# Optimization experiments

Hardware: AMD Instinct MI355X
Metric: run time of the kernel (lower is better)

The kernel has to match this reference:

```python
import jax, jax.numpy as jnp
import numpy as np
import math

FEATURES = 1024; HEADS = 8; STATES = 64; DCONV = 4; EXPAND = 2; NGROUPS = 1; CHUNK = 256
INNER = EXPAND * FEATURES           # 2048
HALF = INNER // 2                   # 1024
HEADDIM = HALF // HEADS             # 128
CONVDIM = HALF + 2 * NGROUPS * STATES  # 1152
B = 2; L = 4096
EPS = 1e-5


def setup_inputs() -> dict:
    key = jax.random.key(0)
    ks = jax.random.split(key, 8)
    u = jax.random.normal(ks[0], (B, L, FEATURES), jnp.float32)
    W_in = jax.random.normal(ks[1], (FEATURES, INNER + 2 * NGROUPS * STATES + HEADS), jnp.float32) * (FEATURES ** -0.5)
    xconv_w = jax.random.normal(ks[2], (CONVDIM, DCONV), jnp.float32) * (DCONV ** -0.5)
    xconv_b = jnp.zeros((CONVDIM,), jnp.float32)
    zconv_w = jax.random.normal(ks[3], (HALF, DCONV), jnp.float32) * (DCONV ** -0.5)
    zconv_b = jnp.zeros((HALF,), jnp.float32)
    dt0 = jnp.exp(jax.random.uniform(ks[4], (HEADS,)) * (math.log(0.1) - math.log(0.001)) + math.log(0.001))
    dt0 = jnp.clip(dt0, 1e-4, None)
    dt_bias = dt0 + jnp.log(-jnp.expm1(-dt0))  # inverse-softplus init
    Alog = jnp.log(jax.random.uniform(ks[5], (HEADS,), minval=1.0, maxval=16.0))
    D = jnp.ones((HEADS,), jnp.float32)
    norm_w = jnp.ones((INNER,), jnp.float32)
    W_out = jax.random.normal(ks[6], (INNER, FEATURES), jnp.float32) * (INNER ** -0.5)
    return dict(u=u, W_in=W_in, xconv_w=xconv_w, xconv_b=xconv_b, zconv_w=zconv_w,
                zconv_b=zconv_b, dt_bias=dt_bias, Alog=Alog, D=D, norm_w=norm_w, W_out=W_out)


def _causal_dwconv_silu(x, w, b):
    # x: (B, L, C), w: (C, K) depthwise, b: (C,) -> causal conv + SiLU, (B, L, C)
    xt = jnp.transpose(x, (0, 2, 1))  # B C L
    kern = w[:, None, :]              # (C, 1, K) -> OIH with groups=C
    y = jax.lax.conv_general_dilated(xt, kern, window_strides=(1,),
                                     padding=[(w.shape[1] - 1, 0)],
                                     dimension_numbers=('NCH', 'OIH', 'NCH'),
                                     feature_group_count=w.shape[0])
    y = jax.nn.silu(y + b[None, :, None])
    return jnp.transpose(y, (0, 2, 1))


def _ssd(x, dt, A, Bm, Cm, Dp, chunk):
    # x:(b,l,h,p) dt:(b,l,h) A:(h,) Bm,Cm:(b,l,g,n) Dp:(h,)
    b, Ltot, H, P = x.shape
    G, N = Bm.shape[2], Bm.shape[3]
    nc = Ltot // chunk
    X = (x * dt[..., None]).reshape(b, nc, chunk, H, P)          # dt-scaled input
    Adt = jnp.transpose((dt * A[None, None, :]).reshape(b, nc, chunk, H), (0, 3, 1, 2))  # b h c k
    Bh = jnp.repeat(Bm, H // G, axis=2).reshape(b, nc, chunk, H, N)
    Ch = jnp.repeat(Cm, H // G, axis=2).reshape(b, nc, chunk, H, N)
    cs = jnp.cumsum(Adt, axis=-1)                                # b h c k
    seg = cs[..., :, None] - cs[..., None, :]                    # b h c l s
    mask = jnp.tril(jnp.ones((chunk, chunk), bool))
    Lmat = jnp.exp(jnp.where(mask, seg, -jnp.inf))               # causal decay matrix
    # intra-chunk (diagonal block) output
    Y_diag = jnp.einsum('bclhn,bcshn,bhcls,bcshp->bclhp', Ch, Bh, Lmat, X)
    # per-chunk final states
    decay_states = jnp.exp(cs[..., -1:] - cs)                    # b h c k
    states = jnp.einsum('bcshn,bhcs,bcshp->bchpn', Bh, decay_states, X)
    chunk_decay = jnp.exp(cs[..., -1])                           # b h c
    def step(carry, inp):
        s, d = inp
        return s + d[..., None, None] * carry, carry             # emit incoming state
    _, prev = jax.lax.scan(step, jnp.zeros((b, H, P, N), x.dtype),
                           (jnp.transpose(states, (1, 0, 2, 3, 4)),
                            jnp.transpose(chunk_decay, (2, 0, 1))))  # prev: (c,b,h,p,n)
    Y_off = jnp.einsum('bclhn,bhcl,cbhpn->bclhp', Ch, jnp.exp(cs), prev)
    Y = (Y_diag + Y_off).reshape(b, Ltot, H, P)
    return Y + Dp[None, None, :, None] * x                       # D skip uses raw x


def _forward(u, W_in, xconv_w, xconv_b, zconv_w, zconv_b, dt_bias, Alog, D, norm_w, W_out):
    zxbcdt = u @ W_in
    z = zxbcdt[..., :HALF]
    xBC = zxbcdt[..., HALF:HALF + CONVDIM]
    dt = jax.nn.softplus(zxbcdt[..., HALF + CONVDIM:] + dt_bias)  # (B,L,H)
    A = -jnp.exp(Alog)
    xBC = _causal_dwconv_silu(xBC, xconv_w, xconv_b)
    z = _causal_dwconv_silu(z, zconv_w, zconv_b)
    x = xBC[..., :HALF].reshape(B, L, HEADS, HEADDIM)
    Bm = xBC[..., HALF:HALF + NGROUPS * STATES].reshape(B, L, NGROUPS, STATES)
    Cm = xBC[..., HALF + NGROUPS * STATES:].reshape(B, L, NGROUPS, STATES)
    y = _ssd(x, dt, A, Bm, Cm, D, CHUNK).reshape(B, L, HALF)
    y = jnp.concatenate([y, z], axis=-1)                          # (B,L,INNER)
    y = y * jax.lax.rsqrt(jnp.mean(y * y, axis=-1, keepdims=True) + EPS) * norm_w
    return y @ W_out


def reference(u, W_in, xconv_w, xconv_b, zconv_w, zconv_b, dt_bias, Alog, D, norm_w, W_out):
    return _forward(u, W_in, xconv_w, xconv_b, zconv_w, zconv_b, dt_bias, Alog, D, norm_w, W_out)
```

## Files before the change

### kernel.cpp

```cpp
#include <hip/hip_runtime.h>
#include <stdint.h>

#define DEV __device__ __forceinline__

typedef __attribute__((ext_vector_type(8))) short bf16x8_t;
typedef __attribute__((ext_vector_type(4))) float f32x4_t;

DEV unsigned short f2bf(float f) {
  union { float f; uint32_t u; } x; x.f = f;
  uint32_t r = x.u + 0x7fffu + ((x.u >> 16) & 1u);
  return (unsigned short)(r >> 16);
}
DEV float bf2f(unsigned short u) {
  union { uint32_t u; float f; } x; x.u = ((uint32_t)u) << 16;
  return x.f;
}

#define GLOAD_LDS16(g, l)                                                              \
  __builtin_amdgcn_global_load_lds((const __attribute__((address_space(1))) unsigned int*)(g), \
                                   (__attribute__((address_space(3))) unsigned int*)(l), 16, 0, 0)

__global__ __launch_bounds__(256) void wdt_kernel(const float* __restrict__ W_in, float* __restrict__ Wdt) {
  int k = blockIdx.x * 256 + threadIdx.x;
  if (k < 1024) {
#pragma unroll
    for (int h = 0; h < 8; ++h)
      Wdt[h * 1024 + k] = W_in[(size_t)k * 2184 + 2176 + h];
  }
}

__global__ __launch_bounds__(256) void uin_kernel(const float* __restrict__ u, const float* __restrict__ Wdt,
                                                  const float* __restrict__ dt_bias,
                                                  unsigned short* __restrict__ A1, float* __restrict__ dtv) {
  int tid = threadIdx.x;
  int row0 = blockIdx.x * 4;
  int lane = tid & 63, wv = tid >> 6;
  float4 w4[8];
#pragma unroll
  for (int h = 0; h < 8; ++h) w4[h] = reinterpret_cast<const float4*>(Wdt + h * 1024)[tid];
  __shared__ float red[4][8];
#pragma unroll
  for (int r = 0; r < 4; ++r) {
    int row = row0 + r;
    float4 v = reinterpret_cast<const float4*>(u + (size_t)row * 1024)[tid];
    ushort4 o;
    o.x = f2bf(v.x); o.y = f2bf(v.y); o.z = f2bf(v.z); o.w = f2bf(v.w);
    reinterpret_cast<ushort4*>(A1 + (size_t)row * 1024)[tid] = o;
    float ps[8];
#pragma unroll
    for (int h = 0; h < 8; ++h)
      ps[h] = v.x * w4[h].x + v.y * w4[h].y + v.z * w4[h].z + v.w * w4[h].w;
#pragma unroll
    for (int h = 0; h < 8; ++h)
#pragma unroll
      for (int off = 32; off > 0; off >>= 1) ps[h] += __shfl_down(ps[h], off, 64);
    if (lane == 0) {
#pragma unroll
      for (int h = 0; h < 8; ++h) red[wv][h] = ps[h];
    }
    __syncthreads();
    if (tid < 8) {
      float s = red[0][tid] + red[1][tid] + red[2][tid] + red[3][tid] + dt_bias[tid];
      float sp = (s > 20.f) ? s : log1pf(expf(s));
      dtv[(size_t)row * 8 + tid] = sp;
    }
    __syncthreads();
  }
}

__global__ void transpose_bf16_kernel(const float* __restrict__ in, unsigned short* __restrict__ out,
                                      int R, int Cin, int stride) {
  __shared__ float t[32][33];
  int bx = blockIdx.x, by = blockIdx.y;
  int tx = threadIdx.x, ty = threadIdx.y;
#pragma unroll
  for (int q = 0; q < 4; ++q) {
    int r = by * 32 + ty + q * 8, c = bx * 32 + tx;
    t[ty + q * 8][tx] = (c < Cin) ? in[(size_t)r * stride + c] : 0.f;
  }
  __syncthreads();
#pragma unroll
  for (int q = 0; q < 4; ++q) {
    int oc = bx * 32 + ty + q * 8;
    int orr = by * 32 + tx;
    out[(size_t)oc * R + orr] = f2bf(t[tx][ty + q * 8]);
  }
}

template <int OBF>
__global__ __launch_bounds__(256) void gemm128_kernel(const unsigned short* __restrict__ A,
                                                      const unsigned short* __restrict__ Bt,
                                                      void* __restrict__ Cout, int K, int ldc, int gx) {
  __shared__ __align__(16) char lds[16384];
  int tid = threadIdx.x, lane = tid & 63, wv = tid >> 6;
  int lr = lane & 15, lk = lane >> 4;
  int wm = wv >> 1, wn = wv & 1;

  int nwg = gridDim.x, lin = blockIdx.x, wg = lin;
  if ((nwg & 7) == 0) { int cpx = nwg >> 3; wg = (lin & 7) * cpx + (lin >> 3); }
  long tileM = (long)(wg % gx) * 128;
  long tileN = (long)(wg / gx) * 128;

  int q0 = wv * 64 + lane;
  int row0 = q0 >> 2;
  int kc = ((q0 & 3) ^ ((row0 >> 1) & 3)) * 8;
  const unsigned short* gA0 = A + (size_t)(tileM + row0) * K + kc;
  const unsigned short* gA1 = A + (size_t)(tileM + row0 + 64) * K + kc;
  const unsigned short* gB0 = Bt + (size_t)(tileN + row0) * K + kc;
  const unsigned short* gB1 = Bt + (size_t)(tileN + row0 + 64) * K + kc;
  char* dA0 = lds + q0 * 16;
  char* dA1 = lds + q0 * 16 + 4096;
  char* dB0 = lds + 8192 + q0 * 16;
  char* dB1 = lds + 8192 + q0 * 16 + 4096;

  int colsw = ((lk ^ ((lr >> 1) & 3)) << 4);

  f32x4_t acc[4][4];
#pragma unroll
  for (int i = 0; i < 4; ++i)
#pragma unroll
    for (int j = 0; j < 4; ++j) acc[i][j] = f32x4_t{0.f, 0.f, 0.f, 0.f};

  for (int k0 = 0; k0 < K; k0 += 32) {
    __syncthreads();
    GLOAD_LDS16(gA0 + k0, dA0);
    GLOAD_LDS16(gA1 + k0, dA1);
    GLOAD_LDS16(gB0 + k0, dB0);
    GLOAD_LDS16(gB1 + k0, dB1);
    __syncthreads();
    bf16x8_t a[4], b[4];
#pragma unroll
    for (int mf = 0; mf < 4; ++mf)
      a[mf] = *reinterpret_cast<const bf16x8_t*>(lds + ((wm * 64 + mf * 16 + lr) << 6) + colsw);
#pragma unroll
    for (int nf = 0; nf < 4; ++nf)
      b[nf] = *reinterpret_cast<const bf16x8_t*>(lds + 8192 + ((wn * 64 + nf * 16 + lr) << 6) + colsw);
#pragma unroll
    for (int mf = 0; mf < 4; ++mf)
#pragma unroll
      for (int nf = 0; nf < 4; ++nf)
        acc[mf][nf] = __builtin_amdgcn_mfma_f32_16x16x32_bf16(a[mf], b[nf], acc[mf][nf], 0, 0, 0);
  }

#pragma unroll
  for (int mf = 0; mf < 4; ++mf)
#pragma unroll
    for (int nf = 0; nf < 4; ++nf) {
      long r0 = tileM + wm * 64 + mf * 16 + lk * 4;
      long c0 = tileN + wn * 64 + nf * 16 + lr;
#pragma unroll
      for (int r = 0; r < 4; ++r) {
        if (OBF)
          ((unsigned short*)Cout)[(size_t)(r0 + r) * ldc + c0] = f2bf(acc[mf][nf][r]);
        else
          ((float*)Cout)[(size_t)(r0 + r) * ldc + c0] = acc[mf][nf][r];
      }
    }
}

template <int C, int IN_STRIDE>
__global__ __launch_bounds__(256) void conv_silu_tile_kernel(const unsigned short* __restrict__ in,
                                                             const float* __restrict__ w,
                                                             const float* __restrict__ bias,
                                                             unsigned short* __restrict__ outp) {
  constexpr int CG = C / 8;
  int idx = blockIdx.x * 256 + threadIdx.x;
  int ch_grp = idx % CG;
  int tb = idx / CG;
  int t0 = (tb & 511) * 8;
  int b = tb >> 9;
  int ch0 = ch_grp * 8;

  float4 wv[8];
#pragma unroll
  for (int e = 0; e < 8; ++e) wv[e] = *reinterpret_cast<const float4*>(w + (ch0 + e) * 4);
  float bs[8];
  {
    float4 b0 = *reinterpret_cast<const float4*>(bias + ch0);
    float4 b1 = *reinterpret_cast<const float4*>(bias + ch0 + 4);
    bs[0] = b0.x; bs[1] = b0.y; bs[2] = b0.z; bs[3] = b0.w;
    bs[4] = b1.x; bs[5] = b1.y; bs[6] = b1.z; bs[7] = b1.w;
  }

  float rows[11][8];
#pragma unroll
  for (int k = 0; k < 11; ++k) {
    int t = t0 - 3 + k;
    if (t >= 0) {
      bf16x8_t v = *reinterpret_cast<const bf16x8_t*>(in + (size_t)((b << 12) + t) * IN_STRIDE + ch0);
#pragma unroll
      for (int e = 0; e < 8; ++e) rows[k][e] = bf2f((unsigned short)v[e]);
    } else {
#pragma unroll
      for (int e = 0; e < 8; ++e) rows[k][e] = 0.f;
    }
  }

#pragma unroll
  for (int tp = 0; tp < 8; ++tp) {
    bf16x8_t o;
#pragma unroll
    for (int e = 0; e < 8; ++e) {
      float a = bs[e] + wv[e].x * rows[tp][e] + wv[e].y * rows[tp + 1][e] +
                wv[e].z * rows[tp + 2][e] + wv[e].w * rows[tp + 3][e];
      a = a / (1.f + expf(-a));
      o[e] = (short)f2bf(a);
    }
    *reinterpret_cast<bf16x8_t*>(outp + (size_t)((b << 12) + t0 + tp) * C + ch0) = o;
  }
}

__global__ __launch_bounds__(256) void ssd1_kernel(const unsigned short* __restrict__ xBC,
                                                   const float* __restrict__ dtv,
                                                   const float* __restrict__ Alog,
                                                   float* __restrict__ csb,
                                                   unsigned short* __restrict__ stat,
                                                   unsigned short* __restrict__ ypart) {
  int blk = blockIdx.x;
  int h = blk & 7, bc = blk >> 3;
  int c = bc & 63, b = bc >> 6;
  int tid = threadIdx.x, lane = tid & 63, wv = tid >> 6;
  int lr = lane & 15, lk = lane >> 4;
  int base = b * 4096 + c * 64;

  __shared__ float csc[64], dts[64], ew[64];
  __shared__ __align__(16) unsigned short Xd[128 * 72];
  __shared__ __align__(16) unsigned short Bnj[64 * 72];
  __shared__ __align__(16) unsigned short Ss[64 * 72];

  if (wv == 0) {
    int j = lane;
    float dt = dtv[(size_t)(base + j) * 8 + h];
    float A = -expf(Alog[h]);
    float s = dt * A;
#pragma unroll
    for (int off = 1; off < 64; off <<= 1) {
      float v = __shfl_up(s, off, 64);
      if (lane >= off) s += v;
    }
    float csl = __shfl(s, 63, 64);
    csc[j] = s; dts[j] = dt; ew[j] = expf(csl - s);
    csb[(size_t)blk * 64 + j] = s;
  }
  __syncthreads();

#pragma unroll
  for (int rr = 0; rr < 4; ++rr) {
    int j = rr * 16 + (tid >> 4);
    int pc = tid & 15;
    bf16x8_t v = *reinterpret_cast<const bf16x8_t*>(xBC + (size_t)(base + j) * 1152 + h * 128 + pc * 8);
    float dj = dts[j];
    int js = j ^ ((pc & 7) << 3);
#pragma unroll
    for (int e = 0; e < 8; ++e) {
      int p = pc * 8 + e;
      Xd[p * 72 + js] = f2bf(bf2f((unsigned short)v[e]) * dj);
    }
  }
#pragma unroll
  for (int rr = 0; rr < 2; ++rr) {
    int j = rr * 32 + (tid >> 3);
    int nc = tid & 7;
    bf16x8_t v = *reinterpret_cast<const bf16x8_t*>(xBC + (size_t)(base + j) * 1152 + 1024 + nc * 8);
    int js = j ^ ((nc & 7) << 3);
#pragma unroll
    for (int e = 0; e < 8; ++e) {
      int n = nc * 8 + e;
      Bnj[n * 72 + js] = (unsigned short)v[e];
    }
  }

  bf16x8_t cf[2];
  {
    size_t crow = (size_t)(base + wv * 16 + lr) * 1152 + 1088;
    cf[0] = *reinterpret_cast<const bf16x8_t*>(xBC + crow + lk * 8);
    cf[1] = *reinterpret_cast<const bf16x8_t*>(xBC + crow + 32 + lk * 8);
  }
  f32x4_t sacc[4];
#pragma unroll
  for (int jf = 0; jf < 4; ++jf) sacc[jf] = f32x4_t{0.f, 0.f, 0.f, 0.f};
#pragma unroll
  for (int ks = 0; ks < 2; ++ks) {
#pragma unroll
    for (int jf = 0; jf < 4; ++jf) {
      bf16x8_t bv = *reinterpret_cast<const bf16x8_t*>(
          xBC + (size_t)(base + jf * 16 + lr) * 1152 + 1024 + ks * 32 + lk * 8);
      sacc[jf] = __builtin_amdgcn_mfma_f32_16x16x32_bf16(cf[ks], bv, sacc[jf], 0, 0, 0);
    }
  }
  __syncthreads();

  {
    float csi[4];
#pragma unroll
    for (int r = 0; r < 4; ++r) csi[r] = csc[wv * 16 + lk * 4 + r];
#pragma unroll
    for (int jf = 0; jf < 4; ++jf) {
      int j = jf * 16 + lr;
      float csj = csc[j];
#pragma unroll
      for (int r = 0; r < 4; ++r) {
        int i = wv * 16 + lk * 4 + r;
        float w = (j <= i) ? expf(csi[r] - csj) : 0.f;
        Ss[i * 72 + j] = f2bf(sacc[jf][r] * w);
      }
    }
  }
  __syncthreads();

  f32x4_t yacc[8];
#pragma unroll
  for (int pf = 0; pf < 8; ++pf) yacc[pf] = f32x4_t{0.f, 0.f, 0.f, 0.f};
  bf16x8_t sa[2];
  sa[0] = *reinterpret_cast<const bf16x8_t*>(Ss + (wv * 16 + lr) * 72 + lk * 8);
  sa[1] = *reinterpret_cast<const bf16x8_t*>(Ss + (wv * 16 + lr) * 72 + 32 + lk * 8);
#pragma unroll
  for (int ks = 0; ks < 2; ++ks) {
    int jb = ks * 32 + lk * 8;
#pragma unroll
    for (int pf = 0; pf < 8; ++pf) {
      int p = pf * 16 + lr;
      bf16x8_t xv = *reinterpret_cast<const bf16x8_t*>(Xd + p * 72 + (jb ^ (((p >> 3) & 7) << 3)));
      yacc[pf] = __builtin_amdgcn_mfma_f32_16x16x32_bf16(sa[ks], xv, yacc[pf], 0, 0, 0);
    }
  }

  f32x4_t st[2][4];
#pragma unroll
  for (int pb = 0; pb < 2; ++pb)
#pragma unroll
    for (int nf = 0; nf < 4; ++nf) st[pb][nf] = f32x4_t{0.f, 0.f, 0.f, 0.f};
#pragma unroll
  for (int pb = 0; pb < 2; ++pb) {
    int p = wv * 32 + pb * 16 + lr;
#pragma unroll
    for (int ks = 0; ks < 2; ++ks) {
      int jb = ks * 32 + lk * 8;
      bf16x8_t xv = *reinterpret_cast<const bf16x8_t*>(Xd + p * 72 + (jb ^ (((p >> 3) & 7) << 3)));
      bf16x8_t xs;
#pragma unroll
      for (int e = 0; e < 8; ++e) xs[e] = (short)f2bf(bf2f((unsigned short)xv[e]) * ew[jb + e]);
#pragma unroll
      for (int nf = 0; nf < 4; ++nf) {
        int n = nf * 16 + lr;
        bf16x8_t bv = *reinterpret_cast<const bf16x8_t*>(Bnj + n * 72 + (jb ^ (((n >> 3) & 7) << 3)));
        st[pb][nf] = __builtin_amdgcn_mfma_f32_16x16x32_bf16(xs, bv, st[pb][nf], 0, 0, 0);
      }
    }
  }

#pragma unroll
  for (int pf = 0; pf < 8; ++pf)
#pragma unroll
    for (int r = 0; r < 4; ++r) {
      int i = wv * 16 + lk * 4 + r;
      ypart[(size_t)(base + i) * 1024 + h * 128 + pf * 16 + lr] = f2bf(yacc[pf][r]);
    }
  unsigned short* so = stat + (size_t)blk * 8192;
#pragma unroll
  for (int pb = 0; pb < 2; ++pb)
#pragma unroll
    for (int nf = 0; nf < 4; ++nf)
#pragma unroll
      for (int r = 0; r < 4; ++r)
        so[(size_t)(wv * 32 + pb * 16 + lk * 4 + r) * 64 + nf * 16 + lr] = f2bf(st[pb][nf][r]);
}

__global__ __launch_bounds__(256) void scan_kernel(const unsigned short* __restrict__ stat,
                                                   const float* __restrict__ csb,
                                                   unsigned short* __restrict__ prevb) {
  int bh = blockIdx.x >> 5;
  int part = blockIdx.x & 31;
  int h = bh & 7, b = bh >> 3;
  int e = part * 256 + threadIdx.x;
  float carry = 0.f;
  for (int c = 0; c < 64; ++c) {
    size_t blk = (size_t)(b * 64 + c) * 8 + h;
    size_t idx = blk * 8192 + e;
    prevb[idx] = f2bf(carry);
    float dec = expf(csb[blk * 64 + 63]);
    carry = bf2f(stat[idx]) + dec * carry;
  }
}

__global__ __launch_bounds__(256) void ssd2_kernel(const unsigned short* __restrict__ xBC,
                                                   const float* __restrict__ csb,
                                                   const unsigned short* __restrict__ prevb,
                                                   const float* __restrict__ Dp,
                                                   const unsigned short* __restrict__ ypart,
                                                   unsigned short* __restrict__ yb) {
  int blk = blockIdx.x;
  int h = blk & 7, bc = blk >> 3;
  int c = bc & 63, b = bc >> 6;
  int tid = threadIdx.x, lane = tid & 63, wv = tid >> 6;
  int lr = lane & 15, lk = lane >> 4;
  int base = b * 4096 + c * 64;
  __shared__ float csc[64];
  if (tid < 64) csc[tid] = csb[(size_t)blk * 64 + tid];
  __syncthreads();

  float sc = expf(csc[wv * 16 + lr]);
  bf16x8_t ca[2];
  {
    size_t crow = (size_t)(base + wv * 16 + lr) * 1152 + 1088;
#pragma unroll
    for (int ks = 0; ks < 2; ++ks) {
      bf16x8_t v = *reinterpret_cast<const bf16x8_t*>(xBC + crow + ks * 32 + lk * 8);
      bf16x8_t d;
#pragma unroll
      for (int e = 0; e < 8; ++e) d[e] = (short)f2bf(bf2f((unsigned short)v[e]) * sc);
      ca[ks] = d;
    }
  }
  f32x4_t acc[8];
#pragma unroll
  for (int pf = 0; pf < 8; ++pf) acc[pf] = f32x4_t{0.f, 0.f, 0.f, 0.f};
#pragma unroll
  for (int ks = 0; ks < 2; ++ks) {
#pragma unroll
    for (int pf = 0; pf < 8; ++pf) {
      bf16x8_t pv = *reinterpret_cast<const bf16x8_t*>(
          prevb + (size_t)blk * 8192 + (size_t)(pf * 16 + lr) * 64 + ks * 32 + lk * 8);
      acc[pf] = __builtin_amdgcn_mfma_f32_16x16x32_bf16(ca[ks], pv, acc[pf], 0, 0, 0);
    }
  }
  float Dh = Dp[h];
#pragma unroll
  for (int pf = 0; pf < 8; ++pf)
#pragma unroll
    for (int r = 0; r < 4; ++r) {
      int i = wv * 16 + lk * 4 + r;
      size_t row = (size_t)(base + i);
      int p = pf * 16 + lr;
      float xr = bf2f(xBC[row * 1152 + h * 128 + p]);
      float yv = bf2f(ypart[row * 1024 + h * 128 + p]) + acc[pf][r] + Dh * xr;
      yb[row * 1024 + h * 128 + p] = f2bf(yv);
    }
}

__global__ __launch_bounds__(256) void rmsnorm_kernel(const unsigned short* __restrict__ y,
                                                      const unsigned short* __restrict__ z,
                                                      const float* __restrict__ nw,
                                                      unsigned short* __restrict__ out) {
  int row = blockIdx.x, tid = threadIdx.x;
  ushort4 ya = reinterpret_cast<const ushort4*>(y + (size_t)row * 1024)[tid];
  ushort4 za = reinterpret_cast<const ushort4*>(z + (size_t)row * 1024)[tid];
  float yf[4] = {bf2f(ya.x), bf2f(ya.y), bf2f(ya.z), bf2f(ya.w)};
  float zf[4] = {bf2f(za.x), bf2f(za.y), bf2f(za.z), bf2f(za.w)};
  float ss = yf[0] * yf[0] + yf[1] * yf[1] + yf[2] * yf[2] + yf[3] * yf[3] +
             zf[0] * zf[0] + zf[1] * zf[1] + zf[2] * zf[2] + zf[3] * zf[3];
#pragma unroll
  for (int off = 32; off > 0; off >>= 1) ss += __shfl_down(ss, off, 64);
  __shared__ float red[4];
  __shared__ float stot;
  int lane = tid & 63, wv = tid >> 6;
  if (lane == 0) red[wv] = ss;
  __syncthreads();
  if (tid == 0) stot = rsqrtf((red[0] + red[1] + red[2] + red[3]) * (1.f / 2048.f) + 1e-5f);
  __syncthreads();
  float s = stot;
  float4 w1 = reinterpret_cast<const float4*>(nw)[tid];
  float4 w2 = reinterpret_cast<const float4*>(nw + 1024)[tid];
  ushort4 o1, o2;
  o1.x = f2bf(yf[0] * s * w1.x); o1.y = f2bf(yf[1] * s * w1.y);
  o1.z = f2bf(yf[2] * s * w1.z); o1.w = f2bf(yf[3] * s * w1.w);
  o2.x = f2bf(zf[0] * s * w2.x); o2.y = f2bf(zf[1] * s * w2.y);
  o2.z = f2bf(zf[2] * s * w2.z); o2.w = f2bf(zf[3] * s * w2.w);
  reinterpret_cast<ushort4*>(out + (size_t)row * 2048)[tid] = o1;
  reinterpret_cast<ushort4*>(out + (size_t)row * 2048 + 1024)[tid] = o2;
}

extern "C" void kernel_launch(void* const* d_in, const int* in_sizes, int n_in,
                              void* d_out, int out_size, void* d_ws, size_t ws_size,
                              hipStream_t stream) {
  const float* u       = (const float*)d_in[0];
  const float* W_in    = (const float*)d_in[1];
  const float* xconv_w = (const float*)d_in[2];
  const float* xconv_b = (const float*)d_in[3];
  const float* zconv_w = (const float*)d_in[4];
  const float* zconv_b = (const float*)d_in[5];
  const float* dt_bias = (const float*)d_in[6];
  const float* Alog    = (const float*)d_in[7];
  const float* Dp      = (const float*)d_in[8];
  const float* norm_w  = (const float*)d_in[9];
  const float* W_out   = (const float*)d_in[10];
  float* out = (float*)d_out;

  char* ws = (char*)d_ws;
  size_t o = 0;
  auto alc = [&](size_t bytes) { void* p = (void*)(ws + o); o = (o + bytes + 255) & ~(size_t)255; return p; };
  char* regA = (char*)alc(16777216);
  unsigned short* Wt1    = (unsigned short*)alc(4456448);
  unsigned short* Wt2    = (unsigned short*)alc(4194304);
  char* regZ = (char*)alc(35651584);
  float*          dtv    = (float*)alc(262144);
  float*          csb    = (float*)alc(262144);
  unsigned short* xBC    = (unsigned short*)alc(18874368);
  unsigned short* zc     = (unsigned short*)alc(16777216);
  char* regS = (char*)alc(33554432);
  unsigned short* prevb  = (unsigned short*)alc(16777216);
  float*          Wdt    = (float*)alc(32768);
  (void)ws_size; (void)in_sizes; (void)n_in; (void)out_size;

  unsigned short* A1     = (unsigned short*)regA;
  unsigned short* yb     = (unsigned short*)regA;
  unsigned short* zx     = (unsigned short*)regZ;
  unsigned short* ypart  = (unsigned short*)regZ;
  unsigned short* stat   = (unsigned short*)regS;
  unsigned short* normed = (unsigned short*)regS;

  dim3 tb(32, 8);
  wdt_kernel<<<4, 256, 0, stream>>>(W_in, Wdt);
  uin_kernel<<<2048, 256, 0, stream>>>(u, Wdt, dt_bias, A1, dtv);
  transpose_bf16_kernel<<<dim3(68, 32), tb, 0, stream>>>(W_in, Wt1, 1024, 2176, 2184);
  transpose_bf16_kernel<<<dim3(32, 64), tb, 0, stream>>>(W_out, Wt2, 2048, 1024, 1024);
  gemm128_kernel<1><<<1088, 256, 0, stream>>>(A1, Wt1, (void*)zx, 1024, 2176, 64);
  conv_silu_tile_kernel<1152, 2176><<<576, 256, 0, stream>>>(zx + 1024, xconv_w, xconv_b, xBC);
  conv_silu_tile_kernel<1024, 2176><<<512, 256, 0, stream>>>(zx, zconv_w, zconv_b, zc);
  ssd1_kernel<<<1024, 256, 0, stream>>>(xBC, dtv, Alog, csb, stat, ypart);
  scan_kernel<<<512, 256, 0, stream>>>(stat, csb, prevb);
  ssd2_kernel<<<1024, 256, 0, stream>>>(xBC, csb, prevb, Dp, ypart, yb);
  rmsnorm_kernel<<<8192, 256, 0, stream>>>(yb, zc, norm_w, normed);
  gemm128_kernel<0><<<512, 256, 0, stream>>>(normed, Wt2, (void*)out, 2048, 1024, 64);
}
```

Before: 247.7 us.

## Double-buffer GEMM with 128x256 tiles, 512 threads and K=64 stages

Replaces the single-buffered 128x128 GEMM with a double-buffered 128x256 tile kernel using 8 waves, a K step of 64, XOR-swizzled LDS layout and s_setprio around the MFMA block. Global-to-LDS loads for the next stage overlap with MFMA work on the current one, and the larger tile raises data reuse. The input projection output is padded to 2304 columns so N divides by 256, which slightly increases work and buffer sizes. Using 96KB of LDS per block limits occupancy.

```diff
diff --git a/kernel.cpp b/kernel.cpp
--- a/kernel.cpp
+++ b/kernel.cpp
@@ -88,32 +88,43 @@
 }
 
 template <int OBF>
-__global__ __launch_bounds__(256) void gemm128_kernel(const unsigned short* __restrict__ A,
+__global__ __launch_bounds__(512) void gemm_db_kernel(const unsigned short* __restrict__ A,
                                                       const unsigned short* __restrict__ Bt,
                                                       void* __restrict__ Cout, int K, int ldc, int gx) {
-  __shared__ __align__(16) char lds[16384];
+  __shared__ __align__(16) char lds[2 * 49152];
   int tid = threadIdx.x, lane = tid & 63, wv = tid >> 6;
   int lr = lane & 15, lk = lane >> 4;
-  int wm = wv >> 1, wn = wv & 1;
+  int wm = wv >> 2, wn = wv & 3;
 
   int nwg = gridDim.x, lin = blockIdx.x, wg = lin;
   if ((nwg & 7) == 0) { int cpx = nwg >> 3; wg = (lin & 7) * cpx + (lin >> 3); }
   long tileM = (long)(wg % gx) * 128;
-  long tileN = (long)(wg / gx) * 128;
-
-  int q0 = wv * 64 + lane;
-  int row0 = q0 >> 2;
-  int kc = ((q0 & 3) ^ ((row0 >> 1) & 3)) * 8;
-  const unsigned short* gA0 = A + (size_t)(tileM + row0) * K + kc;
-  const unsigned short* gA1 = A + (size_t)(tileM + row0 + 64) * K + kc;
-  const unsigned short* gB0 = Bt + (size_t)(tileN + row0) * K + kc;
-  const unsigned short* gB1 = Bt + (size_t)(tileN + row0 + 64) * K + kc;
-  char* dA0 = lds + q0 * 16;
-  char* dA1 = lds + q0 * 16 + 4096;
-  char* dB0 = lds + 8192 + q0 * 16;
-  char* dB1 = lds + 8192 + q0 * 16 + 4096;
-
-  int colsw = ((lk ^ ((lr >> 1) & 3)) << 4);
+  long tileN = (long)(wg / gx) * 256;
+
+  const unsigned short* gAp[2];
+  const unsigned short* gBp[4];
+#pragma unroll
+  for (int i = 0; i < 2; ++i) {
+    int q = tid + i * 512;
+    int row = q >> 3;
+    int c = (q & 7) ^ (row & 7);
+    gAp[i] = A + (size_t)(tileM + row) * K + c * 8;
+  }
+#pragma unroll
+  for (int i = 0; i < 4; ++i) {
+    int q = tid + i * 512;
+    int row = q >> 3;
+    int c = (q & 7) ^ (row & 7);
+    gBp[i] = Bt + (size_t)(tileN + row) * K + c * 8;
+  }
+
+#define STAGE_DB(bsel, kof)                                                                  \
+  do {                                                                                       \
+    _Pragma("unroll") for (int i_ = 0; i_ < 2; ++i_)                                         \
+        GLOAD_LDS16(gAp[i_] + (kof), lds + (bsel) * 49152 + (tid + i_ * 512) * 16);          \
+    _Pragma("unroll") for (int i_ = 0; i_ < 4; ++i_)                                         \
+        GLOAD_LDS16(gBp[i_] + (kof), lds + (bsel) * 49152 + 16384 + (tid + i_ * 512) * 16);  \
+  } while (0)
 
   f32x4_t acc[4][4];
 #pragma unroll
@@ -121,26 +132,45 @@
 #pragma unroll
     for (int j = 0; j < 4; ++j) acc[i][j] = f32x4_t{0.f, 0.f, 0.f, 0.f};
 
-  for (int k0 = 0; k0 < K; k0 += 32) {
-    __syncthreads();
-    GLOAD_LDS16(gA0 + k0, dA0);
-    GLOAD_LDS16(gA1 + k0, dA1);
-    GLOAD_LDS16(gB0 + k0, dB0);
-    GLOAD_LDS16(gB1 + k0, dB1);
-    __syncthreads();
-    bf16x8_t a[4], b[4];
-#pragma unroll
-    for (int mf = 0; mf < 4; ++mf)
-      a[mf] = *reinterpret_cast<const bf16x8_t*>(lds + ((wm * 64 + mf * 16 + lr) << 6) + colsw);
-#pragma unroll
-    for (int nf = 0; nf < 4; ++nf)
-      b[nf] = *reinterpret_cast<const bf16x8_t*>(lds + 8192 + ((wn * 64 + nf * 16 + lr) << 6) + colsw);
-#pragma unroll
-    for (int mf = 0; mf < 4; ++mf)
-#pragma unroll
-      for (int nf = 0; nf < 4; ++nf)
-        acc[mf][nf] = __builtin_amdgcn_mfma_f32_16x16x32_bf16(a[mf], b[nf], acc[mf][nf], 0, 0, 0);
-  }
+  int NT = K >> 6;
+  STAGE_DB(0, 0);
+
+  for (int t = 0; t < NT; ++t) {
+    __builtin_amdgcn_s_barrier();
+    if (t + 1 < NT) {
+      STAGE_DB((t + 1) & 1, (t + 1) * 64);
+      asm volatile("s_waitcnt vmcnt(6)" ::: "memory");
+    } else {
+      asm volatile("s_waitcnt vmcnt(0)" ::: "memory");
+    }
+    __builtin_amdgcn_s_barrier();
+
+    const char* base = lds + (t & 1) * 49152;
+    bf16x8_t bfr[4][2];
+#pragma unroll
+    for (int nf = 0; nf < 4; ++nf) {
+      int row = wn * 64 + nf * 16 + lr;
+#pragma unroll
+      for (int ks = 0; ks < 2; ++ks) {
+        int c = ks * 4 + lk;
+        bfr[nf][ks] = *reinterpret_cast<const bf16x8_t*>(base + 16384 + row * 128 + ((c ^ (row & 7)) << 4));
+      }
+    }
+    __builtin_amdgcn_s_setprio(1);
+#pragma unroll
+    for (int mf = 0; mf < 4; ++mf) {
+      int row = wm * 64 + mf * 16 + lr;
+      bf16x8_t a0 = *reinterpret_cast<const bf16x8_t*>(base + row * 128 + ((lk ^ (row & 7)) << 4));
+      bf16x8_t a1 = *reinterpret_cast<const bf16x8_t*>(base + row * 128 + (((4 + lk) ^ (row & 7)) << 4));
+#pragma unroll
+      for (int nf = 0; nf < 4; ++nf) {
+        acc[mf][nf] = __builtin_amdgcn_mfma_f32_16x16x32_bf16(a0, bfr[nf][0], acc[mf][nf], 0, 0, 0);
+        acc[mf][nf] = __builtin_amdgcn_mfma_f32_16x16x32_bf16(a1, bfr[nf][1], acc[mf][nf], 0, 0, 0);
+      }
+    }
+    __builtin_amdgcn_s_setprio(0);
+  }
+#undef STAGE_DB
 
 #pragma unroll
   for (int mf = 0; mf < 4; ++mf)
@@ -490,9 +520,9 @@
   size_t o = 0;
   auto alc = [&](size_t bytes) { void* p = (void*)(ws + o); o = (o + bytes + 255) & ~(size_t)255; return p; };
   char* regA = (char*)alc(16777216);
-  unsigned short* Wt1    = (unsigned short*)alc(4456448);
+  unsigned short* Wt1    = (unsigned short*)alc(4718592);
   unsigned short* Wt2    = (unsigned short*)alc(4194304);
-  char* regZ = (char*)alc(35651584);
+  char* regZ = (char*)alc(37748736);
   float*          dtv    = (float*)alc(262144);
   float*          csb    = (float*)alc(262144);
   unsigned short* xBC    = (unsigned short*)alc(18874368);
@@ -512,14 +542,14 @@
   dim3 tb(32, 8);
   wdt_kernel<<<4, 256, 0, stream>>>(W_in, Wdt);
   uin_kernel<<<2048, 256, 0, stream>>>(u, Wdt, dt_bias, A1, dtv);
-  transpose_bf16_kernel<<<dim3(68, 32), tb, 0, stream>>>(W_in, Wt1, 1024, 2176, 2184);
+  transpose_bf16_kernel<<<dim3(72, 32), tb, 0, stream>>>(W_in, Wt1, 1024, 2176, 2184);
   transpose_bf16_kernel<<<dim3(32, 64), tb, 0, stream>>>(W_out, Wt2, 2048, 1024, 1024);
-  gemm128_kernel<1><<<1088, 256, 0, stream>>>(A1, Wt1, (void*)zx, 1024, 2176, 64);
-  conv_silu_tile_kernel<1152, 2176><<<576, 256, 0, stream>>>(zx + 1024, xconv_w, xconv_b, xBC);
-  conv_silu_tile_kernel<1024, 2176><<<512, 256, 0, stream>>>(zx, zconv_w, zconv_b, zc);
+  gemm_db_kernel<1><<<576, 512, 0, stream>>>(A1, Wt1, (void*)zx, 1024, 2304, 64);
+  conv_silu_tile_kernel<1152, 2304><<<576, 256, 0, stream>>>(zx + 1024, xconv_w, xconv_b, xBC);
+  conv_silu_tile_kernel<1024, 2304><<<512, 256, 0, stream>>>(zx, zconv_w, zconv_b, zc);
   ssd1_kernel<<<1024, 256, 0, stream>>>(xBC, dtv, Alog, csb, stat, ypart);
   scan_kernel<<<512, 256, 0, stream>>>(stat, csb, prevb);
   ssd2_kernel<<<1024, 256, 0, stream>>>(xBC, csb, prevb, Dp, ypart, yb);
   rmsnorm_kernel<<<8192, 256, 0, stream>>>(yb, zc, norm_w, normed);
-  gemm128_kernel<0><<<512, 256, 0, stream>>>(normed, Wt2, (void*)out, 2048, 1024, 64);
-}
+  gemm_db_kernel<0><<<256, 512, 0, stream>>>(normed, Wt2, (void*)out, 2048, 1024, 64);
+}
```

New measurement: 228.1 us. 7.9% less time.
